# Kernel optimization log

Hardware: AMD Instinct MI355X
Metric: run time of the kernel (lower is better)

The kernel has to match this reference:

```python
import jax, jax.numpy as jnp
import numpy as np

DIM = 1024

def setup_inputs() -> dict:
    key = jax.random.key(0)
    ks = jax.random.split(key, 8)
    B, Sx, Sy, D = 4, 2048, 2048, DIM
    s = 1.0 / np.sqrt(D)
    return {
        "x": jax.random.normal(ks[0], (B, Sx, D), jnp.float32),
        "y": jax.random.normal(ks[1], (B, Sy, D), jnp.float32),
        "Wq": jax.random.normal(ks[2], (D, D), jnp.float32) * s,
        "bq": jnp.zeros((D,), jnp.float32),
        "Wk": jax.random.normal(ks[3], (D, D), jnp.float32) * s,
        "bk": jnp.zeros((D,), jnp.float32),
        "Wv": jax.random.normal(ks[4], (D, D), jnp.float32) * s,
        "bv": jnp.zeros((D,), jnp.float32),
    }

def reference(x, y, Wq, bq, Wk, bk, Wv, bv):
    D = x.shape[-1]
    scale = jnp.sqrt(jnp.asarray(D, x.dtype))
    Q = jnp.einsum('bsd,de->bse', x, Wq) + bq  # [B,Sx,D]
    K = jnp.einsum('btd,de->bte', y, Wk) + bk  # [B,Sy,D]
    V = jnp.einsum('btd,de->bte', y, Wv) + bv  # [B,Sy,D]
    scores = jnp.einsum('bse,bte->bst', Q, K) / scale  # [B,Sx,Sy]
    probs = jax.nn.softmax(scores, axis=-1)
    out = jnp.einsum('bst,bte->bse', probs, V)  # [B,Sx,D]
    return out
```

## Files before the change

### kernel.cpp

```cpp
#include <hip/hip_runtime.h>

typedef __bf16 bf16x8_t __attribute__((ext_vector_type(8)));
typedef float f32x16_t __attribute__((ext_vector_type(16)));
typedef unsigned short ushort_t;

__device__ __forceinline__ unsigned short f2bf(float f) {
  unsigned u = __float_as_uint(f);
  u = (u + 0x7FFFu + ((u >> 16) & 1u)) >> 16;
  return (unsigned short)u;
}
__device__ __forceinline__ float bf2f(unsigned short h) {
  return __uint_as_float(((unsigned)h) << 16);
}

__device__ __forceinline__ void gload16(const void* g, void* l) {
  __builtin_amdgcn_global_load_lds(
      (const __attribute__((address_space(1))) unsigned int*)g,
      (__attribute__((address_space(3))) unsigned int*)l, 16, 0, 0);
}

#define SBAR()                              \
  do {                                      \
    __builtin_amdgcn_s_barrier();           \
    __builtin_amdgcn_sched_barrier(0);      \
  } while (0)
#define VMCNT(N)                                            \
  do {                                                      \
    asm volatile("s_waitcnt vmcnt(" #N ")" ::: "memory");   \
    __builtin_amdgcn_sched_barrier(0);                      \
  } while (0)

template<int EPI, bool OUT_BF16, bool HAS_BIAS>
__global__ __launch_bounds__(256, 3)
void gemm32(const ushort_t* __restrict__ A, const ushort_t* __restrict__ Bt,
            void* __restrict__ Cp, const float* __restrict__ bias,
            float* __restrict__ aux,
            int gx, int gy, int K, int lda, int ldb, int ldc,
            long sA, long sB, long sC, float alpha)
{
  __shared__ __align__(16) ushort_t sm[3 * 8192];
  const int tid = threadIdx.x;
  const int lane = tid & 63;
  const int w = tid >> 6;
  const int wr = w >> 1, wc = w & 1;

  const int per = gridDim.x >> 3;
  int wg = blockIdx.x;
  wg = (wg & 7) * per + (wg >> 3);
  const int bz = wg / (gx * gy);
  const int rr = wg - bz * gx * gy;
  const int by = rr / gx, bx = rr - by * gx;
  const int bm = by * 128, bn = bx * 128;

  const int r0 = (w * 2) * 16 + (lane >> 2);
  const int csw = (((lane & 3) ^ ((r0 >> 1) & 3)) << 3);
  const ushort_t* pA0 = A + (long)bz * sA + (long)(bm + r0) * lda + csw;
  const ushort_t* pA1 = pA0 + 16 * lda;
  const ushort_t* pB0 = Bt + (long)bz * sB + (long)(bn + r0) * ldb + csw;
  const ushort_t* pB1 = pB0 + 16 * ldb;

  auto stage = [&](int kt, int buf) {
    const int k0 = kt << 5;
    ushort_t* s = sm + buf * 8192;
    gload16(pA0 + k0, s + (w * 2) * 512);
    gload16(pA1 + k0, s + (w * 2 + 1) * 512);
    gload16(pB0 + k0, s + 4096 + (w * 2) * 512);
    gload16(pB1 + k0, s + 4096 + (w * 2 + 1) * 512);
  };

  const int l31 = lane & 31, kh = lane >> 5;
  int offA[2][2], offB[2][2];
#pragma unroll
  for (int m = 0; m < 2; ++m) {
    const int row = wr * 64 + m * 32 + l31;
#pragma unroll
    for (int s = 0; s < 2; ++s)
      offA[m][s] = row * 32 + (((s * 2 + kh) ^ ((row >> 1) & 3)) << 3);
  }
#pragma unroll
  for (int n = 0; n < 2; ++n) {
    const int row = wc * 64 + n * 32 + l31;
#pragma unroll
    for (int s = 0; s < 2; ++s)
      offB[n][s] = 4096 + row * 32 + (((s * 2 + kh) ^ ((row >> 1) & 3)) << 3);
  }

  f32x16_t acc[2][2];
#pragma unroll
  for (int m = 0; m < 2; ++m)
#pragma unroll
    for (int n = 0; n < 2; ++n)
#pragma unroll
      for (int i = 0; i < 16; ++i) acc[m][n][i] = 0.f;

  const int nt = K >> 5;
  stage(0, 0);
  if (nt > 1) { stage(1, 1); VMCNT(4); } else { VMCNT(0); }
  SBAR();

#define LDX(off) __builtin_bit_cast(bf16x8_t, *(const uint4*)(sp + (off)))
  int cur = 0, nxt = 1, nn = 2;
  for (int kt = 0; kt < nt; ++kt) {
    if (kt + 2 < nt) stage(kt + 2, nn);
    const ushort_t* sp = sm + cur * 8192;
    bf16x8_t af[2][2], bf[2][2];
#pragma unroll
    for (int m = 0; m < 2; ++m)
#pragma unroll
      for (int s = 0; s < 2; ++s) af[m][s] = LDX(offA[m][s]);
#pragma unroll
    for (int n = 0; n < 2; ++n)
#pragma unroll
      for (int s = 0; s < 2; ++s) bf[n][s] = LDX(offB[n][s]);
    __builtin_amdgcn_s_setprio(1);
#pragma unroll
    for (int s = 0; s < 2; ++s)
#pragma unroll
      for (int m = 0; m < 2; ++m)
#pragma unroll
        for (int n = 0; n < 2; ++n)
          acc[m][n] = __builtin_amdgcn_mfma_f32_32x32x16_bf16(
              af[m][s], bf[n][s], acc[m][n], 0, 0, 0);
    __builtin_amdgcn_s_setprio(0);
    if (kt + 1 < nt) {
      if (kt + 2 < nt) { VMCNT(4); }
      else             { VMCNT(0); }
    }
    SBAR();
    const int tmp = cur; cur = nxt; nxt = nn; nn = tmp;
  }
#undef LDX

  const long zC = (long)bz * sC;
#pragma unroll
  for (int m = 0; m < 2; ++m) {
    const int growb = bm + wr * 64 + m * 32;
    float part[16];
    if constexpr (EPI == 1) {
#pragma unroll
      for (int r = 0; r < 16; ++r) part[r] = 0.f;
    }
#pragma unroll
    for (int n = 0; n < 2; ++n) {
      const int gcol = bn + wc * 64 + n * 32 + l31;
      float bv_ = 0.f;
      if constexpr (HAS_BIAS) bv_ = bias[gcol];
#pragma unroll
      for (int r = 0; r < 16; ++r) {
        const int grow = growb + (r & 3) + 8 * (r >> 2) + 4 * kh;
        float v = acc[m][n][r] * alpha + bv_;
        if constexpr (EPI == 1) {
          const ushort_t pb = f2bf(__expf(v));
          ((ushort_t*)Cp)[zC + (long)grow * ldc + gcol] = pb;
          part[r] += bf2f(pb);
        } else if constexpr (EPI == 2) {
          v *= aux[bz * 2048 + grow];
          ((float*)Cp)[zC + (long)grow * ldc + gcol] = v;
        } else if constexpr (OUT_BF16) {
          ((ushort_t*)Cp)[zC + (long)grow * ldc + gcol] = f2bf(v);
        } else {
          ((float*)Cp)[zC + (long)grow * ldc + gcol] = v;
        }
      }
    }
    if constexpr (EPI == 1) {
#pragma unroll
      for (int step = 1; step < 32; step <<= 1)
#pragma unroll
        for (int r = 0; r < 16; ++r) part[r] += __shfl_xor(part[r], step, 64);
      if (m == 0) {
        __syncthreads();
        float* pf = (float*)sm;
        if (tid < 128) pf[tid] = 0.f;
        __syncthreads();
      }
      if (l31 == 0) {
        float* pf = (float*)sm;
#pragma unroll
        for (int r = 0; r < 16; ++r) {
          const int rloc = wr * 64 + m * 32 + (r & 3) + 8 * (r >> 2) + 4 * kh;
          atomicAdd(&pf[rloc], part[r]);
        }
      }
    }
  }
  if constexpr (EPI == 1) {
    __syncthreads();
    if (tid < 128) {
      const float* pf = (const float*)sm;
      aux[(long)bx * 8192 + bz * 2048 + by * 128 + tid] = pf[tid];
    }
  }
}

__global__ __launch_bounds__(256)
void invrow(const float* __restrict__ psumG, float* __restrict__ inv) {
  const int r = blockIdx.x * 256 + threadIdx.x;
  float s = 0.f;
#pragma unroll
  for (int k = 0; k < 16; ++k) s += psumG[(long)k * 8192 + r];
  inv[r] = 1.0f / s;
}

__global__ __launch_bounds__(256)
void conv2(const float* __restrict__ x, const float* __restrict__ y,
           ushort_t* __restrict__ xb, ushort_t* __restrict__ yb) {
  const int b = blockIdx.x;
  const float* in = (b < 4096) ? x : y;
  ushort_t* out = (b < 4096) ? xb : yb;
  const long i = (long)(b & 4095) * 256 + threadIdx.x;
  const float4 a = ((const float4*)in)[i * 2];
  const float4 c = ((const float4*)in)[i * 2 + 1];
  uint4 o;
  o.x = (unsigned)f2bf(a.x) | ((unsigned)f2bf(a.y) << 16);
  o.y = (unsigned)f2bf(a.z) | ((unsigned)f2bf(a.w) << 16);
  o.z = (unsigned)f2bf(c.x) | ((unsigned)f2bf(c.y) << 16);
  o.w = (unsigned)f2bf(c.z) | ((unsigned)f2bf(c.w) << 16);
  ((uint4*)out)[i] = o;
}

__global__ __launch_bounds__(256)
void wtrans3(const float* __restrict__ W0, const float* __restrict__ W1,
             const float* __restrict__ W2, ushort_t* __restrict__ T0,
             ushort_t* __restrict__ T1, ushort_t* __restrict__ T2) {
  const float* W = (blockIdx.z == 0) ? W0 : (blockIdx.z == 1) ? W1 : W2;
  ushort_t* Wt = (blockIdx.z == 0) ? T0 : (blockIdx.z == 1) ? T1 : T2;
  __shared__ float tile[32][33];
  const int bx = blockIdx.x * 32;
  const int by = blockIdx.y * 32;
  const int t = threadIdx.x;
  const int c = t & 31, r0 = t >> 5;
#pragma unroll
  for (int i = 0; i < 4; ++i)
    tile[r0 + i * 8][c] = W[(long)(by + r0 + i * 8) * 1024 + bx + c];
  __syncthreads();
#pragma unroll
  for (int i = 0; i < 4; ++i)
    Wt[(long)(bx + r0 + i * 8) * 1024 + by + c] = f2bf(tile[c][r0 + i * 8]);
}

__global__ __launch_bounds__(256)
void bconcat(const float* __restrict__ a, const float* __restrict__ b,
             float* __restrict__ o) {
  const int i = blockIdx.x * 256 + threadIdx.x;
  o[i] = (i < 1024) ? a[i] : b[i - 1024];
}

__global__ __launch_bounds__(256)
void transpose_bf16(const ushort_t* __restrict__ in, ushort_t* __restrict__ out,
                    int ld_in, int ld_out, long in_bs, long out_bs) {
  __shared__ ushort_t tt[64][65];
  in += (long)blockIdx.z * in_bs;
  out += (long)blockIdx.z * out_bs;
  const int r0 = blockIdx.y * 64, c0 = blockIdx.x * 64;
  const int tc = threadIdx.x & 31;
  const int tr = threadIdx.x >> 5;
#pragma unroll
  for (int i = 0; i < 8; ++i) {
    const unsigned v = *(const unsigned*)(in + (long)(r0 + tr + 8 * i) * ld_in + c0 + tc * 2);
    tt[tr + 8 * i][tc * 2] = (ushort_t)(v & 0xffff);
    tt[tr + 8 * i][tc * 2 + 1] = (ushort_t)(v >> 16);
  }
  __syncthreads();
#pragma unroll
  for (int i = 0; i < 8; ++i) {
    const unsigned v = (unsigned)tt[tc * 2][tr + 8 * i] |
                       ((unsigned)tt[tc * 2 + 1][tr + 8 * i] << 16);
    *(unsigned*)(out + (long)(c0 + tr + 8 * i) * ld_out + r0 + tc * 2) = v;
  }
}

extern "C" void kernel_launch(void* const* d_in, const int* in_sizes, int n_in,
                              void* d_out, int out_size, void* d_ws, size_t ws_size,
                              hipStream_t stream) {
  const float* x  = (const float*)d_in[0];
  const float* y  = (const float*)d_in[1];
  const float* Wq = (const float*)d_in[2];
  const float* bq = (const float*)d_in[3];
  const float* Wk = (const float*)d_in[4];
  const float* bk = (const float*)d_in[5];
  const float* Wv = (const float*)d_in[6];
  const float* bv = (const float*)d_in[7];
  float* out = (float*)d_out;

  const int D = 1024;
  const long MB_ = 1l << 20;

  ushort_t* ws  = (ushort_t*)d_ws;
  ushort_t* Wqt = ws;
  ushort_t* Wkv = ws + 1 * MB_;
  ushort_t* Wvt = ws + 2 * MB_;
  ushort_t* Qb  = ws + 3 * MB_;
  ushort_t* KV  = ws + 11 * MB_;
  ushort_t* yb  = ws + 27 * MB_;
  ushort_t* Vt  = ws + 27 * MB_;
  ushort_t* xb  = ws + 35 * MB_;
  ushort_t* Sb  = ws + 35 * MB_;
  float*    bkv = (float*)(ws + 51 * MB_);
  float*    psumG = (float*)(ws + 51 * MB_ + 8192);
  float*    inv = psumG + 16 * 8192;

  dim3 blk(256);

  conv2<<<dim3(8192), blk, 0, stream>>>(x, y, xb, yb);
  wtrans3<<<dim3(32, 32, 3), blk, 0, stream>>>(Wq, Wk, Wv, Wqt, Wkv, Wvt);
  bconcat<<<dim3(8), blk, 0, stream>>>(bk, bv, bkv);

  gemm32<0, true, true><<<dim3(512), blk, 0, stream>>>(
      xb, Wqt, Qb, bq, nullptr, 8, 64, D, D, D, D, 0, 0, 0, 1.0f);
  gemm32<0, true, true><<<dim3(1024), blk, 0, stream>>>(
      yb, Wkv, KV, bkv, nullptr, 16, 64, D, D, D, 2048, 0, 0, 0, 1.0f);
  transpose_bf16<<<dim3(16, 32, 4), blk, 0, stream>>>(
      KV + 1024, Vt, 2048, 2048, 2048l * 2048, 1024l * 2048);

  gemm32<1, true, false><<<dim3(1024), blk, 0, stream>>>(
      Qb, KV, Sb, nullptr, psumG, 16, 16, D, D, 2048, 2048,
      2048l * 1024, 2048l * 2048, 2048l * 2048, 0.03125f);

  invrow<<<dim3(32), blk, 0, stream>>>(psumG, inv);

  gemm32<2, false, false><<<dim3(512), blk, 0, stream>>>(
      Sb, Vt, out, nullptr, inv, 8, 16, 2048, 2048, 2048, D,
      2048l * 2048, 1024l * 2048, 2048l * 1024, 1.0f);
}
```

Baseline: 213.2 us.

## Fuse QKV projections into one GEMM and use smaller M tiles with double buffering

Merges the Q and KV projection GEMMs into a single launch over a concatenated weight matrix, picking x or y as the A operand by output column. The GEMM kernel gets an M-tile parameter, so the score and PV GEMMs use 64-row tiles with twice as many blocks. The triple-buffered LDS pipeline with explicit vmcnt waits becomes a simpler double buffer with __syncthreads, and launch bounds are raised for higher occupancy. The extra workgroups may improve load balance, but the simpler pipeline may hide less memory latency and the smaller tiles reduce operand reuse.

```diff
diff --git a/kernel.cpp b/kernel.cpp
--- a/kernel.cpp
+++ b/kernel.cpp
@@ -19,26 +19,18 @@
       (__attribute__((address_space(3))) unsigned int*)l, 16, 0, 0);
 }
 
-#define SBAR()                              \
-  do {                                      \
-    __builtin_amdgcn_s_barrier();           \
-    __builtin_amdgcn_sched_barrier(0);      \
-  } while (0)
-#define VMCNT(N)                                            \
-  do {                                                      \
-    asm volatile("s_waitcnt vmcnt(" #N ")" ::: "memory");   \
-    __builtin_amdgcn_sched_barrier(0);                      \
-  } while (0)
-
-template<int EPI, bool OUT_BF16, bool HAS_BIAS>
-__global__ __launch_bounds__(256, 3)
-void gemm32(const ushort_t* __restrict__ A, const ushort_t* __restrict__ Bt,
+template<int MFR, int EPI, bool OUT_BF16, bool HAS_BIAS>
+__global__ __launch_bounds__(256, (MFR == 2 ? 4 : 6))
+void gemm32(const ushort_t* __restrict__ A, const ushort_t* __restrict__ A2,
+            int nsplit, const ushort_t* __restrict__ Bt,
             void* __restrict__ Cp, const float* __restrict__ bias,
             float* __restrict__ aux,
             int gx, int gy, int K, int lda, int ldb, int ldc,
             long sA, long sB, long sC, float alpha)
 {
-  __shared__ __align__(16) ushort_t sm[3 * 8192];
+  constexpr int ATILE = 2048 * MFR;
+  constexpr int BUFSZ = ATILE + 4096;
+  __shared__ __align__(16) ushort_t sm[2 * BUFSZ];
   const int tid = threadIdx.x;
   const int lane = tid & 63;
   const int w = tid >> 6;
@@ -50,29 +42,33 @@
   const int bz = wg / (gx * gy);
   const int rr = wg - bz * gx * gy;
   const int by = rr / gx, bx = rr - by * gx;
-  const int bm = by * 128, bn = bx * 128;
-
-  const int r0 = (w * 2) * 16 + (lane >> 2);
-  const int csw = (((lane & 3) ^ ((r0 >> 1) & 3)) << 3);
-  const ushort_t* pA0 = A + (long)bz * sA + (long)(bm + r0) * lda + csw;
-  const ushort_t* pA1 = pA0 + 16 * lda;
-  const ushort_t* pB0 = Bt + (long)bz * sB + (long)(bn + r0) * ldb + csw;
-  const ushort_t* pB1 = pB0 + 16 * ldb;
+  const int bm = by * (64 * MFR), bn = bx * 128;
+
+  const ushort_t* Ab = (bn >= nsplit) ? A2 : A;
+
+  const int rA0 = (w * MFR) * 16 + (lane >> 2);
+  const int cswA = (((lane & 3) ^ ((rA0 >> 1) & 3)) << 3);
+  const int rB0 = (w * 2) * 16 + (lane >> 2);
+  const int cswB = (((lane & 3) ^ ((rB0 >> 1) & 3)) << 3);
+  const ushort_t* pA0 = Ab + (long)bz * sA + (long)(bm + rA0) * lda + cswA;
+  const ushort_t* pB0 = Bt + (long)bz * sB + (long)(bn + rB0) * ldb + cswB;
 
   auto stage = [&](int kt, int buf) {
     const int k0 = kt << 5;
-    ushort_t* s = sm + buf * 8192;
-    gload16(pA0 + k0, s + (w * 2) * 512);
-    gload16(pA1 + k0, s + (w * 2 + 1) * 512);
-    gload16(pB0 + k0, s + 4096 + (w * 2) * 512);
-    gload16(pB1 + k0, s + 4096 + (w * 2 + 1) * 512);
+    ushort_t* s = sm + buf * BUFSZ;
+#pragma unroll
+    for (int i = 0; i < MFR; ++i)
+      gload16(pA0 + i * 16 * lda + k0, s + (w * MFR + i) * 512);
+#pragma unroll
+    for (int i = 0; i < 2; ++i)
+      gload16(pB0 + i * 16 * ldb + k0, s + ATILE + (w * 2 + i) * 512);
   };
 
   const int l31 = lane & 31, kh = lane >> 5;
-  int offA[2][2], offB[2][2];
-#pragma unroll
-  for (int m = 0; m < 2; ++m) {
-    const int row = wr * 64 + m * 32 + l31;
+  int offA[MFR][2], offB[2][2];
+#pragma unroll
+  for (int m = 0; m < MFR; ++m) {
+    const int row = wr * (32 * MFR) + m * 32 + l31;
 #pragma unroll
     for (int s = 0; s < 2; ++s)
       offA[m][s] = row * 32 + (((s * 2 + kh) ^ ((row >> 1) & 3)) << 3);
@@ -82,30 +78,29 @@
     const int row = wc * 64 + n * 32 + l31;
 #pragma unroll
     for (int s = 0; s < 2; ++s)
-      offB[n][s] = 4096 + row * 32 + (((s * 2 + kh) ^ ((row >> 1) & 3)) << 3);
-  }
-
-  f32x16_t acc[2][2];
-#pragma unroll
-  for (int m = 0; m < 2; ++m)
+      offB[n][s] = ATILE + row * 32 + (((s * 2 + kh) ^ ((row >> 1) & 3)) << 3);
+  }
+
+  f32x16_t acc[MFR][2];
+#pragma unroll
+  for (int m = 0; m < MFR; ++m)
 #pragma unroll
     for (int n = 0; n < 2; ++n)
 #pragma unroll
       for (int i = 0; i < 16; ++i) acc[m][n][i] = 0.f;
 
+  stage(0, 0);
+  __syncthreads();
+
+#define LDX(off) __builtin_bit_cast(bf16x8_t, *(const uint4*)(sp + (off)))
   const int nt = K >> 5;
-  stage(0, 0);
-  if (nt > 1) { stage(1, 1); VMCNT(4); } else { VMCNT(0); }
-  SBAR();
-
-#define LDX(off) __builtin_bit_cast(bf16x8_t, *(const uint4*)(sp + (off)))
-  int cur = 0, nxt = 1, nn = 2;
   for (int kt = 0; kt < nt; ++kt) {
-    if (kt + 2 < nt) stage(kt + 2, nn);
-    const ushort_t* sp = sm + cur * 8192;
-    bf16x8_t af[2][2], bf[2][2];
-#pragma unroll
-    for (int m = 0; m < 2; ++m)
+    const int cur = kt & 1;
+    if (kt + 1 < nt) stage(kt + 1, cur ^ 1);
+    const ushort_t* sp = sm + cur * BUFSZ;
+    bf16x8_t af[MFR][2], bf[2][2];
+#pragma unroll
+    for (int m = 0; m < MFR; ++m)
 #pragma unroll
       for (int s = 0; s < 2; ++s) af[m][s] = LDX(offA[m][s]);
 #pragma unroll
@@ -116,25 +111,20 @@
 #pragma unroll
     for (int s = 0; s < 2; ++s)
 #pragma unroll
-      for (int m = 0; m < 2; ++m)
+      for (int m = 0; m < MFR; ++m)
 #pragma unroll
         for (int n = 0; n < 2; ++n)
           acc[m][n] = __builtin_amdgcn_mfma_f32_32x32x16_bf16(
               af[m][s], bf[n][s], acc[m][n], 0, 0, 0);
     __builtin_amdgcn_s_setprio(0);
-    if (kt + 1 < nt) {
-      if (kt + 2 < nt) { VMCNT(4); }
-      else             { VMCNT(0); }
-    }
-    SBAR();
-    const int tmp = cur; cur = nxt; nxt = nn; nn = tmp;
+    __syncthreads();
   }
 #undef LDX
 
   const long zC = (long)bz * sC;
 #pragma unroll
-  for (int m = 0; m < 2; ++m) {
-    const int growb = bm + wr * 64 + m * 32;
+  for (int m = 0; m < MFR; ++m) {
+    const int growb = bm + wr * (32 * MFR) + m * 32;
     float part[16];
     if constexpr (EPI == 1) {
 #pragma unroll
@@ -171,14 +161,14 @@
       if (m == 0) {
         __syncthreads();
         float* pf = (float*)sm;
-        if (tid < 128) pf[tid] = 0.f;
+        if (tid < 64 * MFR) pf[tid] = 0.f;
         __syncthreads();
       }
       if (l31 == 0) {
         float* pf = (float*)sm;
 #pragma unroll
         for (int r = 0; r < 16; ++r) {
-          const int rloc = wr * 64 + m * 32 + (r & 3) + 8 * (r >> 2) + 4 * kh;
+          const int rloc = wr * (32 * MFR) + m * 32 + (r & 3) + 8 * (r >> 2) + 4 * kh;
           atomicAdd(&pf[rloc], part[r]);
         }
       }
@@ -186,9 +176,9 @@
   }
   if constexpr (EPI == 1) {
     __syncthreads();
-    if (tid < 128) {
+    if (tid < 64 * MFR) {
       const float* pf = (const float*)sm;
-      aux[(long)bx * 8192 + bz * 2048 + by * 128 + tid] = pf[tid];
+      aux[(long)bx * 8192 + bz * 2048 + by * (64 * MFR) + tid] = pf[tid];
     }
   }
 }
@@ -240,10 +230,10 @@
 }
 
 __global__ __launch_bounds__(256)
-void bconcat(const float* __restrict__ a, const float* __restrict__ b,
-             float* __restrict__ o) {
+void bconcat3(const float* __restrict__ a, const float* __restrict__ b,
+              const float* __restrict__ c, float* __restrict__ o) {
   const int i = blockIdx.x * 256 + threadIdx.x;
-  o[i] = (i < 1024) ? a[i] : b[i - 1024];
+  o[i] = (i < 1024) ? a[i] : (i < 2048) ? b[i - 1024] : c[i - 2048];
 }
 
 __global__ __launch_bounds__(256)
@@ -286,40 +276,40 @@
   const int D = 1024;
   const long MB_ = 1l << 20;
 
-  ushort_t* ws  = (ushort_t*)d_ws;
-  ushort_t* Wqt = ws;
-  ushort_t* Wkv = ws + 1 * MB_;
-  ushort_t* Wvt = ws + 2 * MB_;
-  ushort_t* Qb  = ws + 3 * MB_;
-  ushort_t* KV  = ws + 11 * MB_;
-  ushort_t* yb  = ws + 27 * MB_;
-  ushort_t* Vt  = ws + 27 * MB_;
-  ushort_t* xb  = ws + 35 * MB_;
-  ushort_t* Sb  = ws + 35 * MB_;
-  float*    bkv = (float*)(ws + 51 * MB_);
+  ushort_t* ws   = (ushort_t*)d_ws;
+  ushort_t* Wall = ws;
+  ushort_t* QKV8 = ws + 3 * MB_;
+  ushort_t* Sb   = ws + 27 * MB_;
+  ushort_t* yb   = ws + 27 * MB_;
+  ushort_t* xb   = ws + 35 * MB_;
+  ushort_t* Vt   = ws + 43 * MB_;
+  float*    bias3 = (float*)(ws + 51 * MB_);
   float*    psumG = (float*)(ws + 51 * MB_ + 8192);
-  float*    inv = psumG + 16 * 8192;
+  float*    inv   = psumG + 16 * 8192;
 
   dim3 blk(256);
 
   conv2<<<dim3(8192), blk, 0, stream>>>(x, y, xb, yb);
-  wtrans3<<<dim3(32, 32, 3), blk, 0, stream>>>(Wq, Wk, Wv, Wqt, Wkv, Wvt);
-  bconcat<<<dim3(8), blk, 0, stream>>>(bk, bv, bkv);
-
-  gemm32<0, true, true><<<dim3(512), blk, 0, stream>>>(
-      xb, Wqt, Qb, bq, nullptr, 8, 64, D, D, D, D, 0, 0, 0, 1.0f);
-  gemm32<0, true, true><<<dim3(1024), blk, 0, stream>>>(
-      yb, Wkv, KV, bkv, nullptr, 16, 64, D, D, D, 2048, 0, 0, 0, 1.0f);
+  wtrans3<<<dim3(32, 32, 3), blk, 0, stream>>>(
+      Wq, Wk, Wv, Wall, Wall + 1 * MB_, Wall + 2 * MB_);
+  bconcat3<<<dim3(12), blk, 0, stream>>>(bq, bk, bv, bias3);
+
+  gemm32<2, 0, true, true><<<dim3(1536), blk, 0, stream>>>(
+      xb, yb, 1024, Wall, QKV8, bias3, nullptr,
+      24, 64, D, D, D, 3072, 0, 0, 0, 1.0f);
+
   transpose_bf16<<<dim3(16, 32, 4), blk, 0, stream>>>(
-      KV + 1024, Vt, 2048, 2048, 2048l * 2048, 1024l * 2048);
-
-  gemm32<1, true, false><<<dim3(1024), blk, 0, stream>>>(
-      Qb, KV, Sb, nullptr, psumG, 16, 16, D, D, 2048, 2048,
-      2048l * 1024, 2048l * 2048, 2048l * 2048, 0.03125f);
+      QKV8 + 2048, Vt, 3072, 2048, 2048l * 3072, 1024l * 2048);
+
+  gemm32<1, 1, true, false><<<dim3(2048), blk, 0, stream>>>(
+      QKV8, QKV8, 1 << 30, QKV8 + 1024, Sb, nullptr, psumG,
+      16, 32, D, 3072, 3072, 2048,
+      2048l * 3072, 2048l * 3072, 2048l * 2048, 0.03125f);
 
   invrow<<<dim3(32), blk, 0, stream>>>(psumG, inv);
 
-  gemm32<2, false, false><<<dim3(512), blk, 0, stream>>>(
-      Sb, Vt, out, nullptr, inv, 8, 16, 2048, 2048, 2048, D,
+  gemm32<1, 2, false, false><<<dim3(1024), blk, 0, stream>>>(
+      Sb, Sb, 1 << 30, Vt, out, nullptr, inv,
+      8, 32, 2048, 2048, 2048, D,
       2048l * 2048, 1024l * 2048, 2048l * 1024, 1.0f);
 }
```

Result: slower. 236.5 us (+10.9%).
